# Performance work log

Measured on AMD Instinct MI355X. Metric: run time of the kernel, lower is better.

## Reference

```python
import jax, jax.numpy as jnp
import numpy as np

N_NODES = 50000
N_EDGES = 800000
IN_DIM, HID_DIM, OUT_DIM = 128, 128, 256


def _gcn_conv(x, W, b, src, dst, num_nodes):
    # PyG GCNConv: h = D^{-1/2} (A + I) D^{-1/2} X W + b (self-loops already in src/dst)
    h = x @ W  # (N, F_out)
    ones = jnp.ones(src.shape[0], dtype=h.dtype)
    deg = jax.ops.segment_sum(ones, dst, num_segments=num_nodes)
    dinv = jnp.where(deg > 0, jax.lax.rsqrt(deg), 0.0)
    norm = dinv[src] * dinv[dst]  # (E,)
    msg = h[src] * norm[:, None]  # (E, F_out) gather
    out = jax.ops.segment_sum(msg, dst, num_segments=num_nodes)  # scatter-add
    return out + b


def setup_inputs() -> dict:
    key = jax.random.key(0)
    ks = jax.random.split(key, 6)
    x = jax.random.normal(ks[0], (N_NODES, IN_DIM), dtype=jnp.float32)
    edge_index = jax.random.randint(ks[1], (2, N_EDGES), 0, N_NODES, dtype=jnp.int64)
    W1 = jax.random.normal(ks[2], (IN_DIM, HID_DIM), dtype=jnp.float32) / np.sqrt(IN_DIM)
    b1 = jnp.zeros((HID_DIM,), jnp.float32)
    W2 = jax.random.normal(ks[3], (HID_DIM, OUT_DIM), dtype=jnp.float32) / np.sqrt(HID_DIM)
    b2 = jnp.zeros((OUT_DIM,), jnp.float32)
    Wa = jax.random.normal(ks[4], (OUT_DIM, 1), dtype=jnp.float32) / np.sqrt(OUT_DIM)
    ba = jnp.zeros((1,), jnp.float32)
    return {"x": x, "edge_index": edge_index, "W1": W1, "b1": b1, "W2": W2, "b2": b2, "Wa": Wa, "ba": ba}


def reference(x, edge_index, W1, b1, W2, b2, Wa, ba):
    n = x.shape[0]
    loops = jnp.arange(n, dtype=edge_index.dtype)
    src = jnp.concatenate([edge_index[0], loops])
    dst = jnp.concatenate([edge_index[1], loops])
    h = jax.nn.relu(_gcn_conv(x, W1, b1, src, dst, n))
    # dropout is a no-op in eval mode
    node_embeddings = jax.nn.relu(_gcn_conv(h, W2, b2, src, dst, n))
    logits = node_embeddings @ Wa + ba  # (N, 1)
    attn = jax.nn.softmax(logits, axis=0)  # softmax over nodes
    graph_embedding = jnp.sum(node_embeddings * attn, axis=0, keepdims=True)  # (1, OUT_DIM)
    return (node_embeddings, graph_embedding)
```

## Files before the change

### kernel.cpp

```cpp
#include <hip/hip_runtime.h>
#include <hip/hip_fp16.h>
#include <math.h>

typedef __attribute__((ext_vector_type(8))) short bf16x8;
typedef __attribute__((ext_vector_type(4))) float f32x4;

static __device__ __forceinline__ unsigned short f2bf(float x) {
    unsigned u = __float_as_uint(x);
    unsigned r = (u + 0x7FFF + ((u >> 16) & 1)) >> 16;
    return (unsigned short)r;
}
static __device__ __forceinline__ float bf2f(unsigned short h) {
    return __uint_as_float(((unsigned)h) << 16);
}
static __device__ __forceinline__ void addh8(float a[8], uint4 v) {
    float2 f;
    f = __half22float2(*(const __half2*)&v.x); a[0] += f.x; a[1] += f.y;
    f = __half22float2(*(const __half2*)&v.y); a[2] += f.x; a[3] += f.y;
    f = __half22float2(*(const __half2*)&v.z); a[4] += f.x; a[5] += f.y;
    f = __half22float2(*(const __half2*)&v.w); a[6] += f.x; a[7] += f.y;
}
static __device__ __forceinline__ void gll16(const unsigned short* g, unsigned short* l) {
    __builtin_amdgcn_global_load_lds(
        (const __attribute__((address_space(1))) unsigned int*)(const void*)g,
        (__attribute__((address_space(3))) unsigned int*)(void*)l, 16, 0, 0);
}


__global__ __launch_bounds__(256) void count_deg_kernel(const int* __restrict__ dst, int E,
                                                        int* __restrict__ deg,
                                                        int* __restrict__ epos) {
    int e = blockIdx.x * 256 + threadIdx.x;
    if (e < E) epos[e] = atomicAdd(&deg[dst[e]], 1);
}

__global__ __launch_bounds__(256) void scan_partial_kernel(const int* __restrict__ deg, int n,
                                                           int* __restrict__ partials) {
    int idx = blockIdx.x * 1024 + threadIdx.x * 4;
    int4 v = make_int4(0, 0, 0, 0);
    if (idx + 3 < n) v = *(const int4*)(deg + idx);
    else {
        if (idx < n) v.x = deg[idx];
        if (idx + 1 < n) v.y = deg[idx + 1];
        if (idx + 2 < n) v.z = deg[idx + 2];
    }
    int s = v.x + v.y + v.z + v.w;
    for (int off = 1; off < 64; off <<= 1) s += __shfl_xor(s, off);
    __shared__ int sm[4];
    int wave = threadIdx.x >> 6;
    if ((threadIdx.x & 63) == 0) sm[wave] = s;
    __syncthreads();
    if (threadIdx.x == 0) partials[blockIdx.x] = sm[0] + sm[1] + sm[2] + sm[3];
}

__global__ __launch_bounds__(256) void scan_final_kernel(const int* __restrict__ deg, int n,
                                                         const int* __restrict__ partials, int nbk,
                                                         int* __restrict__ rowptr) {
    int idx = blockIdx.x * 1024 + threadIdx.x * 4;
    int4 v = make_int4(0, 0, 0, 0);
    if (idx + 3 < n) v = *(const int4*)(deg + idx);
    else {
        if (idx < n) v.x = deg[idx];
        if (idx + 1 < n) v.y = deg[idx + 1];
        if (idx + 2 < n) v.z = deg[idx + 2];
    }
    int tsum = v.x + v.y + v.z + v.w;
    int lane = threadIdx.x & 63, wave = threadIdx.x >> 6;
    int s = tsum;
    for (int off = 1; off < 64; off <<= 1) {
        int u = __shfl_up(s, off);
        if (lane >= off) s += u;
    }
    __shared__ int wsum[4];
    __shared__ int bb;
    if (lane == 63) wsum[wave] = s;
    if (threadIdx.x < 64) {
        int pv = (threadIdx.x < nbk) ? partials[threadIdx.x] : 0;
        int ps = pv;
        for (int off = 1; off < 64; off <<= 1) {
            int u = __shfl_up(ps, off);
            if (threadIdx.x >= off) ps += u;
        }
        if (threadIdx.x == blockIdx.x) bb = ps - pv;
        if (blockIdx.x == 0 && threadIdx.x == 63) rowptr[n] = ps;
    }
    __syncthreads();
    int base = bb;
    for (int w = 0; w < wave; ++w) base += wsum[w];
    int e0 = base + s - tsum;
    int4 o;
    o.x = e0; o.y = e0 + v.x; o.z = o.y + v.y; o.w = o.z + v.z;
    if (idx + 3 < n) *(int4*)(rowptr + idx) = o;
    else {
        if (idx < n) rowptr[idx] = o.x;
        if (idx + 1 < n) rowptr[idx + 1] = o.y;
        if (idx + 2 < n) rowptr[idx + 2] = o.z;
    }
}


__global__ __launch_bounds__(256) void prep_kernel(
    const int* __restrict__ src, const int* __restrict__ dst, const int* __restrict__ epos, int E,
    const int* __restrict__ rowptr, int* __restrict__ csrsrc, int scatterBlocks,
    const float* __restrict__ x, float* __restrict__ dinv,
    __half2* __restrict__ xs16, int n, int prescaleBlocks,
    const float* __restrict__ W1, const float* __restrict__ W2,
    unsigned short* __restrict__ w1h, unsigned short* __restrict__ w1l,
    unsigned short* __restrict__ w2h, unsigned short* __restrict__ w2l) {
    int b = blockIdx.x;
    if (b < scatterBlocks) {
        int e = b * 256 + threadIdx.x;
        if (e < E) csrsrc[rowptr[dst[e]] + epos[e]] = src[e];
    } else if (b < scatterBlocks + prescaleBlocks) {
        int node = (b - scatterBlocks) * 4 + (threadIdx.x >> 6);
        int lane = threadIdx.x & 63;
        if (node >= n) return;
        float di = rsqrtf((float)(rowptr[node + 1] - rowptr[node] + 1));
        if (lane == 0) dinv[node] = di;
        float2 v = *(const float2*)(x + (size_t)node * 128 + (lane << 1));
        xs16[(size_t)node * 64 + lane] = __floats2half2_rn(di * v.x, di * v.y);
    } else {
        int i = (b - scatterBlocks - prescaleBlocks) * 256 + threadIdx.x;
        if (i < 128 * 128) {
            int nn = i >> 7, k = i & 127;
            float v = W1[k * 128 + nn];
            unsigned short h = f2bf(v);
            int kp = (k & 64) + ((((k >> 3) & 7) ^ (nn & 7)) << 3) + (k & 7);
            w1h[nn * 128 + kp] = h;
            w1l[nn * 128 + kp] = f2bf(v - bf2f(h));
        } else if (i < 128 * 128 + 256 * 128) {
            int j = i - 128 * 128;
            int nn = j >> 7, k = j & 127;
            float v = W2[k * 256 + nn];
            unsigned short h = f2bf(v);
            int kp = (k & 64) + ((((k >> 3) & 7) ^ (nn & 7)) << 3) + (k & 7);
            w2h[nn * 128 + kp] = h;
            w2l[nn * 128 + kp] = f2bf(v - bf2f(h));
        }
    }
}


__global__ __launch_bounds__(256) void aggregate_kernel(const unsigned short* __restrict__ X16,
                                                        const float* __restrict__ dinv,
                                                        const int* __restrict__ rowptr,
                                                        const int* __restrict__ csrsrc,
                                                        unsigned short* __restrict__ outH,
                                                        unsigned short* __restrict__ outL, int n) {
    int node = blockIdx.x * 16 + (threadIdx.x >> 4);
    int sl = threadIdx.x & 15;
    if (node >= n) return;
    const uint4* Xv = (const uint4*)X16;
    float acc[8] = {0.f, 0.f, 0.f, 0.f, 0.f, 0.f, 0.f, 0.f};
    addh8(acc, Xv[(size_t)node * 16 + sl]);
    int e0 = rowptr[node];
    int e1 = rowptr[node + 1];
    int e = e0;
    for (; e + 4 <= e1; e += 4) {
        int s0 = csrsrc[e], s1 = csrsrc[e + 1], s2 = csrsrc[e + 2], s3 = csrsrc[e + 3];
        uint4 v0 = Xv[(size_t)s0 * 16 + sl];
        uint4 v1 = Xv[(size_t)s1 * 16 + sl];
        uint4 v2 = Xv[(size_t)s2 * 16 + sl];
        uint4 v3 = Xv[(size_t)s3 * 16 + sl];
        addh8(acc, v0); addh8(acc, v1); addh8(acc, v2); addh8(acc, v3);
    }
    for (; e < e1; ++e) {
        uint4 v = Xv[(size_t)csrsrc[e] * 16 + sl];
        addh8(acc, v);
    }
    float di = dinv[node];
    unsigned short h[8], l[8];
#pragma unroll
    for (int j = 0; j < 8; ++j) {
        float f = di * acc[j];
        h[j] = f2bf(f);
        l[j] = f2bf(f - bf2f(h[j]));
    }
    uint4 hv, lv;
    hv.x = (unsigned)h[0] | ((unsigned)h[1] << 16);
    hv.y = (unsigned)h[2] | ((unsigned)h[3] << 16);
    hv.z = (unsigned)h[4] | ((unsigned)h[5] << 16);
    hv.w = (unsigned)h[6] | ((unsigned)h[7] << 16);
    lv.x = (unsigned)l[0] | ((unsigned)l[1] << 16);
    lv.y = (unsigned)l[2] | ((unsigned)l[3] << 16);
    lv.z = (unsigned)l[4] | ((unsigned)l[5] << 16);
    lv.w = (unsigned)l[6] | ((unsigned)l[7] << 16);
    int pos = ((sl & 8) | ((sl & 7) ^ (node & 7))) * 8;
    *(uint4*)(outH + (size_t)node * 128 + pos) = hv;
    *(uint4*)(outL + (size_t)node * 128 + pos) = lv;
}


template <int N, bool SCALE_DINV, bool DO_LOGITS, bool OUT_F16>
__global__ __launch_bounds__(256, 2) void gemm_mfma(const unsigned short* __restrict__ Ah,
                                                    const unsigned short* __restrict__ Al,
                                                    const unsigned short* __restrict__ Bth,
                                                    const unsigned short* __restrict__ Btl,
                                                    const float* __restrict__ bias,
                                                    void* __restrict__ Cout, int M,
                                                    const float* __restrict__ dinv,
                                                    const float* __restrict__ Wa,
                                                    float* __restrict__ logits) {
    __shared__ unsigned short AsH[128 * 64];
    __shared__ unsigned short AsL[128 * 64];
    __shared__ unsigned short BsH[128 * 64];
    __shared__ unsigned short BsL[128 * 64];

    const int t = threadIdx.x;
    const int lane = t & 63;
    const int wave = t >> 6;
    const int wrow = wave >> 1;
    const int wcol = wave & 1;
    const int lq = lane >> 4;
    const int lm = lane & 15;
    const int row0 = blockIdx.x * 128;
    const int col0 = blockIdx.y * 128;

    const int lr = lane >> 3;
    const int p8 = (lane & 7) * 8;

    f32x4 acc[4][4] = {};
    float lacc[4][4] = {};

    for (int kc = 0; kc < 2; ++kc) {
        __syncthreads();
#pragma unroll
        for (int j = 0; j < 4; ++j) {
            int seg = wave * 4 + j;
            int r = seg * 8 + lr;
            size_t goA = (size_t)(row0 + r) * 128 + kc * 64 + p8;
            size_t goB = (size_t)(col0 + r) * 128 + kc * 64 + p8;
            gll16(Ah + goA, AsH + seg * 512);
            gll16(Al + goA, AsL + seg * 512);
            gll16(Bth + goB, BsH + seg * 512);
            gll16(Btl + goB, BsL + seg * 512);
        }
        __syncthreads();

#pragma unroll
        for (int ks = 0; ks < 2; ++ks) {
            bf16x8 ah[4], al[4], bh[4], bl[4];
            int gbase = ks * 4 + lq;
#pragma unroll
            for (int rt = 0; rt < 4; ++rt) {
                int ra = wrow * 64 + rt * 16 + lm;
                int off = ra * 64 + (gbase ^ (ra & 7)) * 8;
                ah[rt] = *(const bf16x8*)(AsH + off);
                al[rt] = *(const bf16x8*)(AsL + off);
            }
#pragma unroll
            for (int ct = 0; ct < 4; ++ct) {
                int nb = wcol * 64 + ct * 16 + lm;
                int off = nb * 64 + (gbase ^ (nb & 7)) * 8;
                bh[ct] = *(const bf16x8*)(BsH + off);
                bl[ct] = *(const bf16x8*)(BsL + off);
            }
#pragma unroll
            for (int rt = 0; rt < 4; ++rt)
#pragma unroll
                for (int ct = 0; ct < 4; ++ct) {
                    acc[rt][ct] = __builtin_amdgcn_mfma_f32_16x16x32_bf16(ah[rt], bh[ct], acc[rt][ct], 0, 0, 0);
                    acc[rt][ct] = __builtin_amdgcn_mfma_f32_16x16x32_bf16(al[rt], bh[ct], acc[rt][ct], 0, 0, 0);
                    acc[rt][ct] = __builtin_amdgcn_mfma_f32_16x16x32_bf16(ah[rt], bl[ct], acc[rt][ct], 0, 0, 0);
                }
        }
    }

#pragma unroll
    for (int ct = 0; ct < 4; ++ct) {
        int col = col0 + wcol * 64 + ct * 16 + lm;
        float bc = bias[col];
        float wac = DO_LOGITS ? Wa[col] : 0.f;
#pragma unroll
        for (int rt = 0; rt < 4; ++rt) {
            int rowb = row0 + wrow * 64 + rt * 16 + lq * 4;
#pragma unroll
            for (int reg = 0; reg < 4; ++reg) {
                int gr = rowb + reg;
                if (gr < M) {
                    float o = fmaxf(acc[rt][ct][reg] + bc, 0.f);
                    if (SCALE_DINV) o *= dinv[gr];
                    if (OUT_F16) ((__half*)Cout)[(size_t)gr * N + col] = __float2half(o);
                    else ((float*)Cout)[(size_t)gr * N + col] = o;
                    if (DO_LOGITS) lacc[rt][reg] += o * wac;
                }
            }
        }
    }

    if (DO_LOGITS) {
#pragma unroll
        for (int rt = 0; rt < 4; ++rt)
#pragma unroll
            for (int reg = 0; reg < 4; ++reg) {
                float s = lacc[rt][reg];
                s += __shfl_xor(s, 1);
                s += __shfl_xor(s, 2);
                s += __shfl_xor(s, 4);
                s += __shfl_xor(s, 8);
                int gr = row0 + wrow * 64 + rt * 16 + lq * 4 + reg;
                if (lm == 0 && gr < M) atomicAdd(&logits[gr], s);
            }
    }
}


__global__ __launch_bounds__(256) void maxsum_kernel(const float* __restrict__ logits, int n,
                                                     float2* __restrict__ part,
                                                     float* __restrict__ outTail) {
    if (blockIdx.x == 0) outTail[threadIdx.x] = 0.f;
    float m = -INFINITY, s = 0.f;
    for (int i = blockIdx.x * 256 + threadIdx.x; i < n; i += gridDim.x * 256) {
        float v = logits[i];
        if (v > m) { s = s * expf(m - v) + 1.f; m = v; }
        else s += expf(v - m);
    }
    __shared__ float sm[256], ss[256];
    sm[threadIdx.x] = m; ss[threadIdx.x] = s;
    __syncthreads();
    for (int off = 128; off > 0; off >>= 1) {
        if (threadIdx.x < off) {
            float m1 = sm[threadIdx.x], s1 = ss[threadIdx.x];
            float m2 = sm[threadIdx.x + off], s2 = ss[threadIdx.x + off];
            float M = fmaxf(m1, m2);
            sm[threadIdx.x] = M;
            ss[threadIdx.x] = s1 * expf(m1 - M) + s2 * expf(m2 - M);
        }
        __syncthreads();
    }
    if (threadIdx.x == 0) part[blockIdx.x] = make_float2(sm[0], ss[0]);
}

static __device__ __forceinline__ float2 merge_part(const float2* __restrict__ part, int t,
                                                    float* red2) {
    if (t < 64) {
        float2 p = part[t];
        float m = p.x, s = p.y;
        for (int off = 32; off > 0; off >>= 1) {
            float m2 = __shfl_xor(m, off);
            float s2 = __shfl_xor(s, off);
            float M = fmaxf(m, m2);
            s = s * expf(m - M) + s2 * expf(m2 - M);
            m = M;
        }
        if (t == 0) { red2[0] = m; red2[1] = s; }
    }
    __syncthreads();
    return make_float2(red2[0], red2[1]);
}

__global__ __launch_bounds__(256) void weighted_sum_kernel(const float* __restrict__ emb,
                                                           const float* __restrict__ logits,
                                                           const float2* __restrict__ part,
                                                           float* __restrict__ gpart, int n) {
    __shared__ float red2[2];
    float g = merge_part(part, threadIdx.x, red2).x;
    int wave = threadIdx.x >> 6;
    int lane = threadIdx.x & 63;
    int stride = gridDim.x * 4;
    float4 acc = make_float4(0.f, 0.f, 0.f, 0.f);
#pragma unroll 2
    for (int r = blockIdx.x * 4 + wave; r < n; r += stride) {
        float w = expf(logits[r] - g);
        float4 v = *(const float4*)(emb + (size_t)r * 256 + (lane << 2));
        acc.x += w * v.x; acc.y += w * v.y; acc.z += w * v.z; acc.w += w * v.w;
    }
    __shared__ float4 sm[256];
    sm[threadIdx.x] = acc;
    __syncthreads();
    if (wave == 0) {
        float4 a = sm[lane], b = sm[64 + lane], c = sm[128 + lane], d = sm[192 + lane];
        float4 s;
        s.x = (a.x + b.x) + (c.x + d.x);
        s.y = (a.y + b.y) + (c.y + d.y);
        s.z = (a.z + b.z) + (c.z + d.z);
        s.w = (a.w + b.w) + (c.w + d.w);
        *(float4*)(gpart + (size_t)blockIdx.x * 256 + (lane << 2)) = s;
    }
}

__global__ __launch_bounds__(256) void reduce_gpart_kernel(const float* __restrict__ gpart,
                                                           const float2* __restrict__ part,
                                                           float* __restrict__ outTail, int nb) {
    __shared__ float red2[2];
    float gsum = merge_part(part, threadIdx.x, red2).y;
    int rows = nb / gridDim.x;
    int r0 = blockIdx.x * rows;
    float s = 0.f;
    for (int r = r0; r < r0 + rows; ++r) s += gpart[(size_t)r * 256 + threadIdx.x];
    atomicAdd(&outTail[threadIdx.x], s / gsum);
}


extern "C" void kernel_launch(void* const* d_in, const int* in_sizes, int n_in,
                              void* d_out, int out_size, void* d_ws, size_t ws_size,
                              hipStream_t stream) {
    const float* x  = (const float*)d_in[0];
    const int* ei   = (const int*)d_in[1];
    const float* W1 = (const float*)d_in[2];
    const float* b1 = (const float*)d_in[3];
    const float* W2 = (const float*)d_in[4];
    const float* b2 = (const float*)d_in[5];
    const float* Wa = (const float*)d_in[6];
    float* out = (float*)d_out;

    const int n = in_sizes[0] / 128;
    const int E = in_sizes[1] / 2;
    const int* srcA = ei;
    const int* dstA = ei + E;
    const int nb = (n + 1023) / 1024;
    const int WS_BLOCKS = 1024;

    unsigned short* xs16 = (unsigned short*)d_ws;
    unsigned short* aggH = xs16 + (size_t)n * 128;
    unsigned short* aggL = aggH + (size_t)n * 128;
    unsigned short* w1h  = aggL + (size_t)n * 128;
    unsigned short* w1l  = w1h + 128 * 128;
    unsigned short* w2h  = w1l + 128 * 128;
    unsigned short* w2l  = w2h + 256 * 128;
    float* dinv   = (float*)(w2l + 256 * 128);
    float* logits = dinv + n;
    int* deg      = (int*)(logits + n);
    int* rowptr   = deg + n;
    int* partials = rowptr + n + 1;
    float2* part  = (float2*)(partials + 64);
    float* gpart  = (float*)(part + 64);
    int* epos     = (int*)(gpart + WS_BLOCKS * 256);
    int* csrsrc   = epos + E;

    hipMemsetAsync(logits, 0, sizeof(float) * (size_t)(2 * n), stream);

    count_deg_kernel<<<(E + 255) / 256, 256, 0, stream>>>(dstA, E, deg, epos);
    scan_partial_kernel<<<nb, 256, 0, stream>>>(deg, n, partials);
    scan_final_kernel<<<nb, 256, 0, stream>>>(deg, n, partials, nb, rowptr);

    int scatterBlocks = (E + 255) / 256;
    int prescaleBlocks = (n + 3) / 4;
    int wconvBlocks = (128 * 128 + 256 * 128 + 255) / 256;
    prep_kernel<<<scatterBlocks + prescaleBlocks + wconvBlocks, 256, 0, stream>>>(
        srcA, dstA, epos, E, rowptr, csrsrc, scatterBlocks,
        x, dinv, (__half2*)xs16, n, prescaleBlocks,
        W1, W2, w1h, w1l, w2h, w2l);

    int aggBlocks = (n + 15) / 16;
    int gemmRows = (n + 127) / 128;

    aggregate_kernel<<<aggBlocks, 256, 0, stream>>>(xs16, dinv, rowptr, csrsrc, aggH, aggL, n);
    gemm_mfma<128, true, false, true><<<dim3(gemmRows, 1), 256, 0, stream>>>(
        aggH, aggL, w1h, w1l, b1, xs16, n, dinv, nullptr, nullptr);
    aggregate_kernel<<<aggBlocks, 256, 0, stream>>>(xs16, dinv, rowptr, csrsrc, aggH, aggL, n);
    gemm_mfma<256, false, true, false><<<dim3(gemmRows, 2), 256, 0, stream>>>(
        aggH, aggL, w2h, w2l, b2, out, n, nullptr, Wa, logits);

    maxsum_kernel<<<64, 256, 0, stream>>>(logits, n, part, out + (size_t)n * 256);
    weighted_sum_kernel<<<WS_BLOCKS, 256, 0, stream>>>(out, logits, part, gpart, n);
    reduce_gpart_kernel<<<32, 256, 0, stream>>>(gpart, part, out + (size_t)n * 256, WS_BLOCKS);
}
```

Baseline: 291.7 us.

## Fuse neighbor aggregation into MFMA GEMM, staging aggregated rows in LDS

Each GCN layer's CSR gather-aggregate now runs inside the GEMM kernel. A 512-thread block aggregates 128 rows into split bf16 hi/lo LDS tiles, then multiplies them by weights read directly from global memory instead of staged through LDS. This removes the aggH/aggL round-trip through global memory and two kernel launches. The layer-2 GEMM now covers all 256 columns per block instead of splitting them across two blocks, so each block loads more weight data and gets less column parallelism. The gather phase also uses only four threads per node with wide per-thread accumulators, which may raise register pressure and reduce memory-level parallelism.

Result: no change. 296.8 us (+1.7%).

```diff
diff --git a/kernel.cpp b/kernel.cpp
--- a/kernel.cpp
+++ b/kernel.cpp
@@ -13,17 +13,12 @@
 static __device__ __forceinline__ float bf2f(unsigned short h) {
     return __uint_as_float(((unsigned)h) << 16);
 }
-static __device__ __forceinline__ void addh8(float a[8], uint4 v) {
+static __device__ __forceinline__ void addh8(float* a, uint4 v) {
     float2 f;
     f = __half22float2(*(const __half2*)&v.x); a[0] += f.x; a[1] += f.y;
     f = __half22float2(*(const __half2*)&v.y); a[2] += f.x; a[3] += f.y;
     f = __half22float2(*(const __half2*)&v.z); a[4] += f.x; a[5] += f.y;
     f = __half22float2(*(const __half2*)&v.w); a[6] += f.x; a[7] += f.y;
-}
-static __device__ __forceinline__ void gll16(const unsigned short* g, unsigned short* l) {
-    __builtin_amdgcn_global_load_lds(
-        (const __attribute__((address_space(1))) unsigned int*)(const void*)g,
-        (__attribute__((address_space(3))) unsigned int*)(void*)l, 16, 0, 0);
 }
 
 
@@ -125,150 +120,135 @@
             int nn = i >> 7, k = i & 127;
             float v = W1[k * 128 + nn];
             unsigned short h = f2bf(v);
-            int kp = (k & 64) + ((((k >> 3) & 7) ^ (nn & 7)) << 3) + (k & 7);
-            w1h[nn * 128 + kp] = h;
-            w1l[nn * 128 + kp] = f2bf(v - bf2f(h));
+            w1h[nn * 128 + k] = h;
+            w1l[nn * 128 + k] = f2bf(v - bf2f(h));
         } else if (i < 128 * 128 + 256 * 128) {
             int j = i - 128 * 128;
             int nn = j >> 7, k = j & 127;
             float v = W2[k * 256 + nn];
             unsigned short h = f2bf(v);
-            int kp = (k & 64) + ((((k >> 3) & 7) ^ (nn & 7)) << 3) + (k & 7);
-            w2h[nn * 128 + kp] = h;
-            w2l[nn * 128 + kp] = f2bf(v - bf2f(h));
-        }
-    }
-}
-
-
-__global__ __launch_bounds__(256) void aggregate_kernel(const unsigned short* __restrict__ X16,
-                                                        const float* __restrict__ dinv,
-                                                        const int* __restrict__ rowptr,
-                                                        const int* __restrict__ csrsrc,
-                                                        unsigned short* __restrict__ outH,
-                                                        unsigned short* __restrict__ outL, int n) {
-    int node = blockIdx.x * 16 + (threadIdx.x >> 4);
-    int sl = threadIdx.x & 15;
-    if (node >= n) return;
-    const uint4* Xv = (const uint4*)X16;
-    float acc[8] = {0.f, 0.f, 0.f, 0.f, 0.f, 0.f, 0.f, 0.f};
-    addh8(acc, Xv[(size_t)node * 16 + sl]);
-    int e0 = rowptr[node];
-    int e1 = rowptr[node + 1];
-    int e = e0;
-    for (; e + 4 <= e1; e += 4) {
-        int s0 = csrsrc[e], s1 = csrsrc[e + 1], s2 = csrsrc[e + 2], s3 = csrsrc[e + 3];
-        uint4 v0 = Xv[(size_t)s0 * 16 + sl];
-        uint4 v1 = Xv[(size_t)s1 * 16 + sl];
-        uint4 v2 = Xv[(size_t)s2 * 16 + sl];
-        uint4 v3 = Xv[(size_t)s3 * 16 + sl];
-        addh8(acc, v0); addh8(acc, v1); addh8(acc, v2); addh8(acc, v3);
-    }
-    for (; e < e1; ++e) {
-        uint4 v = Xv[(size_t)csrsrc[e] * 16 + sl];
-        addh8(acc, v);
-    }
-    float di = dinv[node];
-    unsigned short h[8], l[8];
-#pragma unroll
-    for (int j = 0; j < 8; ++j) {
-        float f = di * acc[j];
-        h[j] = f2bf(f);
-        l[j] = f2bf(f - bf2f(h[j]));
-    }
-    uint4 hv, lv;
-    hv.x = (unsigned)h[0] | ((unsigned)h[1] << 16);
-    hv.y = (unsigned)h[2] | ((unsigned)h[3] << 16);
-    hv.z = (unsigned)h[4] | ((unsigned)h[5] << 16);
-    hv.w = (unsigned)h[6] | ((unsigned)h[7] << 16);
-    lv.x = (unsigned)l[0] | ((unsigned)l[1] << 16);
-    lv.y = (unsigned)l[2] | ((unsigned)l[3] << 16);
-    lv.z = (unsigned)l[4] | ((unsigned)l[5] << 16);
-    lv.w = (unsigned)l[6] | ((unsigned)l[7] << 16);
-    int pos = ((sl & 8) | ((sl & 7) ^ (node & 7))) * 8;
-    *(uint4*)(outH + (size_t)node * 128 + pos) = hv;
-    *(uint4*)(outL + (size_t)node * 128 + pos) = lv;
-}
-
-
-template <int N, bool SCALE_DINV, bool DO_LOGITS, bool OUT_F16>
-__global__ __launch_bounds__(256, 2) void gemm_mfma(const unsigned short* __restrict__ Ah,
-                                                    const unsigned short* __restrict__ Al,
-                                                    const unsigned short* __restrict__ Bth,
-                                                    const unsigned short* __restrict__ Btl,
-                                                    const float* __restrict__ bias,
-                                                    void* __restrict__ Cout, int M,
-                                                    const float* __restrict__ dinv,
-                                                    const float* __restrict__ Wa,
-                                                    float* __restrict__ logits) {
-    __shared__ unsigned short AsH[128 * 64];
-    __shared__ unsigned short AsL[128 * 64];
-    __shared__ unsigned short BsH[128 * 64];
-    __shared__ unsigned short BsL[128 * 64];
+            w2h[nn * 128 + k] = h;
+            w2l[nn * 128 + k] = f2bf(v - bf2f(h));
+        }
+    }
+}
+
+
+template <int NCOLS, bool SCALE_DINV, bool DO_LOGITS, bool OUT_F16>
+__global__ __launch_bounds__(512, 2) void fused_gemm(
+    const unsigned short* __restrict__ X16,
+    const int* __restrict__ rowptr, const int* __restrict__ csrsrc,
+    const float* __restrict__ dinv,
+    const unsigned short* __restrict__ Bth, const unsigned short* __restrict__ Btl,
+    const float* __restrict__ bias, void* __restrict__ Cout, int M,
+    const float* __restrict__ Wa, float* __restrict__ logits) {
+    constexpr int CT = NCOLS / 64;
+    __shared__ unsigned short AsH[128 * 128];
+    __shared__ unsigned short AsL[128 * 128];
 
     const int t = threadIdx.x;
+    const int row0 = blockIdx.x * 128;
+
+    {
+        const int nl = t >> 2;
+        const int sub = t & 3;
+        const int row = row0 + nl;
+        float acc[32];
+#pragma unroll
+        for (int i = 0; i < 32; ++i) acc[i] = 0.f;
+        float di = 0.f;
+        if (row < M) {
+            const uint4* __restrict__ Xv = (const uint4*)X16;
+            size_t sb = (size_t)row * 16 + sub * 4;
+            uint4 v0 = Xv[sb], v1 = Xv[sb + 1], v2 = Xv[sb + 2], v3 = Xv[sb + 3];
+            addh8(acc, v0); addh8(acc + 8, v1); addh8(acc + 16, v2); addh8(acc + 24, v3);
+            int e1 = rowptr[row + 1];
+            int e = rowptr[row];
+            for (; e + 2 <= e1; e += 2) {
+                int s0 = csrsrc[e], s1 = csrsrc[e + 1];
+                size_t b0 = (size_t)s0 * 16 + sub * 4;
+                size_t b1 = (size_t)s1 * 16 + sub * 4;
+                uint4 a0 = Xv[b0], a1 = Xv[b0 + 1], a2 = Xv[b0 + 2], a3 = Xv[b0 + 3];
+                uint4 c0 = Xv[b1], c1 = Xv[b1 + 1], c2 = Xv[b1 + 2], c3 = Xv[b1 + 3];
+                addh8(acc, a0); addh8(acc + 8, a1); addh8(acc + 16, a2); addh8(acc + 24, a3);
+                addh8(acc, c0); addh8(acc + 8, c1); addh8(acc + 16, c2); addh8(acc + 24, c3);
+            }
+            if (e < e1) {
+                size_t b0 = (size_t)csrsrc[e] * 16 + sub * 4;
+                uint4 a0 = Xv[b0], a1 = Xv[b0 + 1], a2 = Xv[b0 + 2], a3 = Xv[b0 + 3];
+                addh8(acc, a0); addh8(acc + 8, a1); addh8(acc + 16, a2); addh8(acc + 24, a3);
+            }
+            di = dinv[row];
+        }
+#pragma unroll
+        for (int j = 0; j < 4; ++j) {
+            int ga = sub * 4 + j;
+            int off = nl * 128 + (ga >> 3) * 64 + (((ga & 7) ^ (nl & 7)) << 3);
+            unsigned short h[8], l[8];
+#pragma unroll
+            for (int q = 0; q < 8; ++q) {
+                float f = di * acc[j * 8 + q];
+                h[q] = f2bf(f);
+                l[q] = f2bf(f - bf2f(h[q]));
+            }
+            uint4 hv, lv;
+            hv.x = (unsigned)h[0] | ((unsigned)h[1] << 16);
+            hv.y = (unsigned)h[2] | ((unsigned)h[3] << 16);
+            hv.z = (unsigned)h[4] | ((unsigned)h[5] << 16);
+            hv.w = (unsigned)h[6] | ((unsigned)h[7] << 16);
+            lv.x = (unsigned)l[0] | ((unsigned)l[1] << 16);
+            lv.y = (unsigned)l[2] | ((unsigned)l[3] << 16);
+            lv.z = (unsigned)l[4] | ((unsigned)l[5] << 16);
+            lv.w = (unsigned)l[6] | ((unsigned)l[7] << 16);
+            *(uint4*)(AsH + off) = hv;
+            *(uint4*)(AsL + off) = lv;
+        }
+    }
+    __syncthreads();
+
     const int lane = t & 63;
     const int wave = t >> 6;
-    const int wrow = wave >> 1;
-    const int wcol = wave & 1;
+    const int wrow = wave >> 2;
+    const int wcol = wave & 3;
     const int lq = lane >> 4;
     const int lm = lane & 15;
-    const int row0 = blockIdx.x * 128;
-    const int col0 = blockIdx.y * 128;
-
-    const int lr = lane >> 3;
-    const int p8 = (lane & 7) * 8;
-
-    f32x4 acc[4][4] = {};
+
+    f32x4 acc2[4][CT] = {};
     float lacc[4][4] = {};
 
-    for (int kc = 0; kc < 2; ++kc) {
-        __syncthreads();
-#pragma unroll
-        for (int j = 0; j < 4; ++j) {
-            int seg = wave * 4 + j;
-            int r = seg * 8 + lr;
-            size_t goA = (size_t)(row0 + r) * 128 + kc * 64 + p8;
-            size_t goB = (size_t)(col0 + r) * 128 + kc * 64 + p8;
-            gll16(Ah + goA, AsH + seg * 512);
-            gll16(Al + goA, AsL + seg * 512);
-            gll16(Bth + goB, BsH + seg * 512);
-            gll16(Btl + goB, BsL + seg * 512);
-        }
-        __syncthreads();
-
+#pragma unroll
+    for (int kc = 0; kc < 2; ++kc)
 #pragma unroll
         for (int ks = 0; ks < 2; ++ks) {
-            bf16x8 ah[4], al[4], bh[4], bl[4];
-            int gbase = ks * 4 + lq;
+            const int gbase = ks * 4 + lq;
+            bf16x8 ah[4], al[4], bh[CT], bl[CT];
 #pragma unroll
             for (int rt = 0; rt < 4; ++rt) {
                 int ra = wrow * 64 + rt * 16 + lm;
-                int off = ra * 64 + (gbase ^ (ra & 7)) * 8;
+                int off = ra * 128 + kc * 64 + ((gbase ^ (ra & 7)) << 3);
                 ah[rt] = *(const bf16x8*)(AsH + off);
                 al[rt] = *(const bf16x8*)(AsL + off);
             }
 #pragma unroll
-            for (int ct = 0; ct < 4; ++ct) {
-                int nb = wcol * 64 + ct * 16 + lm;
-                int off = nb * 64 + (gbase ^ (nb & 7)) * 8;
-                bh[ct] = *(const bf16x8*)(BsH + off);
-                bl[ct] = *(const bf16x8*)(BsL + off);
+            for (int ct = 0; ct < CT; ++ct) {
+                int col = wcol * (16 * CT) + ct * 16 + lm;
+                size_t bo = (size_t)col * 128 + kc * 64 + gbase * 8;
+                bh[ct] = *(const bf16x8*)(Bth + bo);
+                bl[ct] = *(const bf16x8*)(Btl + bo);
             }
 #pragma unroll
             for (int rt = 0; rt < 4; ++rt)
 #pragma unroll
-                for (int ct = 0; ct < 4; ++ct) {
-                    acc[rt][ct] = __builtin_amdgcn_mfma_f32_16x16x32_bf16(ah[rt], bh[ct], acc[rt][ct], 0, 0, 0);
-                    acc[rt][ct] = __builtin_amdgcn_mfma_f32_16x16x32_bf16(al[rt], bh[ct], acc[rt][ct], 0, 0, 0);
-                    acc[rt][ct] = __builtin_amdgcn_mfma_f32_16x16x32_bf16(ah[rt], bl[ct], acc[rt][ct], 0, 0, 0);
+                for (int ct = 0; ct < CT; ++ct) {
+                    acc2[rt][ct] = __builtin_amdgcn_mfma_f32_16x16x32_bf16(ah[rt], bh[ct], acc2[rt][ct], 0, 0, 0);
+                    acc2[rt][ct] = __builtin_amdgcn_mfma_f32_16x16x32_bf16(al[rt], bh[ct], acc2[rt][ct], 0, 0, 0);
+                    acc2[rt][ct] = __builtin_amdgcn_mfma_f32_16x16x32_bf16(ah[rt], bl[ct], acc2[rt][ct], 0, 0, 0);
                 }
         }
-    }
-
-#pragma unroll
-    for (int ct = 0; ct < 4; ++ct) {
-        int col = col0 + wcol * 64 + ct * 16 + lm;
+
+#pragma unroll
+    for (int ct = 0; ct < CT; ++ct) {
+        int col = wcol * (16 * CT) + ct * 16 + lm;
         float bc = bias[col];
         float wac = DO_LOGITS ? Wa[col] : 0.f;
 #pragma unroll
@@ -278,10 +258,10 @@
             for (int reg = 0; reg < 4; ++reg) {
                 int gr = rowb + reg;
                 if (gr < M) {
-                    float o = fmaxf(acc[rt][ct][reg] + bc, 0.f);
+                    float o = fmaxf(acc2[rt][ct][reg] + bc, 0.f);
                     if (SCALE_DINV) o *= dinv[gr];
-                    if (OUT_F16) ((__half*)Cout)[(size_t)gr * N + col] = __float2half(o);
-                    else ((float*)Cout)[(size_t)gr * N + col] = o;
+                    if (OUT_F16) ((__half*)Cout)[(size_t)gr * NCOLS + col] = __float2half(o);
+                    else ((float*)Cout)[(size_t)gr * NCOLS + col] = o;
                     if (DO_LOGITS) lacc[rt][reg] += o * wac;
                 }
             }
@@ -412,9 +392,8 @@
     const int WS_BLOCKS = 1024;
 
     unsigned short* xs16 = (unsigned short*)d_ws;
-    unsigned short* aggH = xs16 + (size_t)n * 128;
-    unsigned short* aggL = aggH + (size_t)n * 128;
-    unsigned short* w1h  = aggL + (size_t)n * 128;
+    unsigned short* h16  = xs16 + (size_t)n * 128;
+    unsigned short* w1h  = h16 + (size_t)n * 128;
     unsigned short* w1l  = w1h + 128 * 128;
     unsigned short* w2h  = w1l + 128 * 128;
     unsigned short* w2l  = w2h + 256 * 128;
@@ -442,15 +421,12 @@
         x, dinv, (__half2*)xs16, n, prescaleBlocks,
         W1, W2, w1h, w1l, w2h, w2l);
 
-    int aggBlocks = (n + 15) / 16;
     int gemmRows = (n + 127) / 128;
 
-    aggregate_kernel<<<aggBlocks, 256, 0, stream>>>(xs16, dinv, rowptr, csrsrc, aggH, aggL, n);
-    gemm_mfma<128, true, false, true><<<dim3(gemmRows, 1), 256, 0, stream>>>(
-        aggH, aggL, w1h, w1l, b1, xs16, n, dinv, nullptr, nullptr);
-    aggregate_kernel<<<aggBlocks, 256, 0, stream>>>(xs16, dinv, rowptr, csrsrc, aggH, aggL, n);
-    gemm_mfma<256, false, true, false><<<dim3(gemmRows, 2), 256, 0, stream>>>(
-        aggH, aggL, w2h, w2l, b2, out, n, nullptr, Wa, logits);
+    fused_gemm<128, true, false, true><<<gemmRows, 512, 0, stream>>>(
+        xs16, rowptr, csrsrc, dinv, w1h, w1l, b1, h16, n, nullptr, nullptr);
+    fused_gemm<256, false, true, false><<<gemmRows, 512, 0, stream>>>(
+        h16, rowptr, csrsrc, dinv, w2h, w2l, b2, out, n, Wa, logits);
 
     maxsum_kernel<<<64, 256, 0, stream>>>(logits, n, part, out + (size_t)n * 256);
     weighted_sum_kernel<<<WS_BLOCKS, 256, 0, stream>>>(out, logits, part, gpart, n);
```

## Split fp16 feature table into column chunks and aggregate chunk-by-chunk

Applied to the files above, without the earlier changes.

The fp16 node-feature table is stored as four column-chunk planes of 32 halves each, written both by the prescale step and by the layer-1 GEMM epilogue. Aggregation now runs as four separate launches, one per chunk, so each gathered working set (about 3.2 MB) can stay resident in L2/LLC during the random neighbor gathers. Each launch re-reads the CSR arrays, and the index loads are marked nontemporal and unrolled by eight. The cost is four times the CSR index traffic, more kernel launches, and a strided GEMM output write pattern.

Measured after the change: 350.1 us. +20.0%, slower.

```diff
diff --git a/kernel.cpp b/kernel.cpp
--- a/kernel.cpp
+++ b/kernel.cpp
@@ -13,7 +13,7 @@
 static __device__ __forceinline__ float bf2f(unsigned short h) {
     return __uint_as_float(((unsigned)h) << 16);
 }
-static __device__ __forceinline__ void addh8(float a[8], uint4 v) {
+static __device__ __forceinline__ void addh8(float* a, uint4 v) {
     float2 f;
     f = __half22float2(*(const __half2*)&v.x); a[0] += f.x; a[1] += f.y;
     f = __half22float2(*(const __half2*)&v.y); a[2] += f.x; a[3] += f.y;
@@ -103,7 +103,7 @@
     const int* __restrict__ src, const int* __restrict__ dst, const int* __restrict__ epos, int E,
     const int* __restrict__ rowptr, int* __restrict__ csrsrc, int scatterBlocks,
     const float* __restrict__ x, float* __restrict__ dinv,
-    __half2* __restrict__ xs16, int n, int prescaleBlocks,
+    __half2* __restrict__ xs16c, int n, int prescaleBlocks,
     const float* __restrict__ W1, const float* __restrict__ W2,
     unsigned short* __restrict__ w1h, unsigned short* __restrict__ w1l,
     unsigned short* __restrict__ w2h, unsigned short* __restrict__ w2l) {
@@ -118,7 +118,8 @@
         float di = rsqrtf((float)(rowptr[node + 1] - rowptr[node] + 1));
         if (lane == 0) dinv[node] = di;
         float2 v = *(const float2*)(x + (size_t)node * 128 + (lane << 1));
-        xs16[(size_t)node * 64 + lane] = __floats2half2_rn(di * v.x, di * v.y);
+        xs16c[((size_t)(lane >> 4) * n + node) * 16 + (lane & 15)] =
+            __floats2half2_rn(di * v.x, di * v.y);
     } else {
         int i = (b - scatterBlocks - prescaleBlocks) * 256 + threadIdx.x;
         if (i < 128 * 128) {
@@ -141,40 +142,61 @@
 }
 
 
-__global__ __launch_bounds__(256) void aggregate_kernel(const unsigned short* __restrict__ X16,
-                                                        const float* __restrict__ dinv,
-                                                        const int* __restrict__ rowptr,
-                                                        const int* __restrict__ csrsrc,
-                                                        unsigned short* __restrict__ outH,
-                                                        unsigned short* __restrict__ outL, int n) {
-    int node = blockIdx.x * 16 + (threadIdx.x >> 4);
-    int sl = threadIdx.x & 15;
+__global__ __launch_bounds__(256) void agg_chunk_kernel(
+    const unsigned short* __restrict__ X16c, const int* __restrict__ rowptr,
+    const int* __restrict__ csrsrc, const float* __restrict__ dinv,
+    unsigned short* __restrict__ outH, unsigned short* __restrict__ outL,
+    int n, int chunk) {
+    int node = blockIdx.x * 64 + (threadIdx.x >> 2);
+    int sub = threadIdx.x & 3;
     if (node >= n) return;
-    const uint4* Xv = (const uint4*)X16;
+    const uint4* __restrict__ Xv = (const uint4*)X16c + (size_t)chunk * n * 4;
     float acc[8] = {0.f, 0.f, 0.f, 0.f, 0.f, 0.f, 0.f, 0.f};
-    addh8(acc, Xv[(size_t)node * 16 + sl]);
-    int e0 = rowptr[node];
+    addh8(acc, Xv[(size_t)node * 4 + sub]);
+    int e = rowptr[node];
     int e1 = rowptr[node + 1];
-    int e = e0;
+    for (; e + 8 <= e1; e += 8) {
+        int s0 = __builtin_nontemporal_load(csrsrc + e);
+        int s1 = __builtin_nontemporal_load(csrsrc + e + 1);
+        int s2 = __builtin_nontemporal_load(csrsrc + e + 2);
+        int s3 = __builtin_nontemporal_load(csrsrc + e + 3);
+        int s4 = __builtin_nontemporal_load(csrsrc + e + 4);
+        int s5 = __builtin_nontemporal_load(csrsrc + e + 5);
+        int s6 = __builtin_nontemporal_load(csrsrc + e + 6);
+        int s7 = __builtin_nontemporal_load(csrsrc + e + 7);
+        uint4 v0 = Xv[(size_t)s0 * 4 + sub];
+        uint4 v1 = Xv[(size_t)s1 * 4 + sub];
+        uint4 v2 = Xv[(size_t)s2 * 4 + sub];
+        uint4 v3 = Xv[(size_t)s3 * 4 + sub];
+        uint4 v4 = Xv[(size_t)s4 * 4 + sub];
+        uint4 v5 = Xv[(size_t)s5 * 4 + sub];
+        uint4 v6 = Xv[(size_t)s6 * 4 + sub];
+        uint4 v7 = Xv[(size_t)s7 * 4 + sub];
+        addh8(acc, v0); addh8(acc, v1); addh8(acc, v2); addh8(acc, v3);
+        addh8(acc, v4); addh8(acc, v5); addh8(acc, v6); addh8(acc, v7);
+    }
     for (; e + 4 <= e1; e += 4) {
-        int s0 = csrsrc[e], s1 = csrsrc[e + 1], s2 = csrsrc[e + 2], s3 = csrsrc[e + 3];
-        uint4 v0 = Xv[(size_t)s0 * 16 + sl];
-        uint4 v1 = Xv[(size_t)s1 * 16 + sl];
-        uint4 v2 = Xv[(size_t)s2 * 16 + sl];
-        uint4 v3 = Xv[(size_t)s3 * 16 + sl];
+        int s0 = __builtin_nontemporal_load(csrsrc + e);
+        int s1 = __builtin_nontemporal_load(csrsrc + e + 1);
+        int s2 = __builtin_nontemporal_load(csrsrc + e + 2);
+        int s3 = __builtin_nontemporal_load(csrsrc + e + 3);
+        uint4 v0 = Xv[(size_t)s0 * 4 + sub];
+        uint4 v1 = Xv[(size_t)s1 * 4 + sub];
+        uint4 v2 = Xv[(size_t)s2 * 4 + sub];
+        uint4 v3 = Xv[(size_t)s3 * 4 + sub];
         addh8(acc, v0); addh8(acc, v1); addh8(acc, v2); addh8(acc, v3);
     }
     for (; e < e1; ++e) {
-        uint4 v = Xv[(size_t)csrsrc[e] * 16 + sl];
-        addh8(acc, v);
+        int s0 = __builtin_nontemporal_load(csrsrc + e);
+        addh8(acc, Xv[(size_t)s0 * 4 + sub]);
     }
     float di = dinv[node];
     unsigned short h[8], l[8];
 #pragma unroll
-    for (int j = 0; j < 8; ++j) {
-        float f = di * acc[j];
-        h[j] = f2bf(f);
-        l[j] = f2bf(f - bf2f(h[j]));
+    for (int q = 0; q < 8; ++q) {
+        float f = di * acc[q];
+        h[q] = f2bf(f);
+        l[q] = f2bf(f - bf2f(h[q]));
     }
     uint4 hv, lv;
     hv.x = (unsigned)h[0] | ((unsigned)h[1] << 16);
@@ -185,7 +207,8 @@
     lv.y = (unsigned)l[2] | ((unsigned)l[3] << 16);
     lv.z = (unsigned)l[4] | ((unsigned)l[5] << 16);
     lv.w = (unsigned)l[6] | ((unsigned)l[7] << 16);
-    int pos = ((sl & 8) | ((sl & 7) ^ (node & 7))) * 8;
+    int ga = chunk * 4 + sub;
+    int pos = ((ga & 8) | ((ga & 7) ^ (node & 7))) * 8;
     *(uint4*)(outH + (size_t)node * 128 + pos) = hv;
     *(uint4*)(outL + (size_t)node * 128 + pos) = lv;
 }
@@ -280,7 +303,8 @@
                 if (gr < M) {
                     float o = fmaxf(acc[rt][ct][reg] + bc, 0.f);
                     if (SCALE_DINV) o *= dinv[gr];
-                    if (OUT_F16) ((__half*)Cout)[(size_t)gr * N + col] = __float2half(o);
+                    if (OUT_F16)
+                        ((__half*)Cout)[((size_t)(col >> 5) * M + gr) * 32 + (col & 31)] = __float2half(o);
                     else ((float*)Cout)[(size_t)gr * N + col] = o;
                     if (DO_LOGITS) lacc[rt][reg] += o * wac;
                 }
@@ -411,13 +435,13 @@
     const int nb = (n + 1023) / 1024;
     const int WS_BLOCKS = 1024;
 
-    unsigned short* xs16 = (unsigned short*)d_ws;
-    unsigned short* aggH = xs16 + (size_t)n * 128;
-    unsigned short* aggL = aggH + (size_t)n * 128;
-    unsigned short* w1h  = aggL + (size_t)n * 128;
-    unsigned short* w1l  = w1h + 128 * 128;
-    unsigned short* w2h  = w1l + 128 * 128;
-    unsigned short* w2l  = w2h + 256 * 128;
+    unsigned short* xs16c = (unsigned short*)d_ws;
+    unsigned short* aggH  = xs16c + (size_t)n * 128;
+    unsigned short* aggL  = aggH + (size_t)n * 128;
+    unsigned short* w1h   = aggL + (size_t)n * 128;
+    unsigned short* w1l   = w1h + 128 * 128;
+    unsigned short* w2h   = w1l + 128 * 128;
+    unsigned short* w2l   = w2h + 256 * 128;
     float* dinv   = (float*)(w2l + 256 * 128);
     float* logits = dinv + n;
     int* deg      = (int*)(logits + n);
@@ -439,16 +463,19 @@
     int wconvBlocks = (128 * 128 + 256 * 128 + 255) / 256;
     prep_kernel<<<scatterBlocks + prescaleBlocks + wconvBlocks, 256, 0, stream>>>(
         srcA, dstA, epos, E, rowptr, csrsrc, scatterBlocks,
-        x, dinv, (__half2*)xs16, n, prescaleBlocks,
+        x, dinv, (__half2*)xs16c, n, prescaleBlocks,
         W1, W2, w1h, w1l, w2h, w2l);
 
-    int aggBlocks = (n + 15) / 16;
+    int NB = (n + 63) / 64;
     int gemmRows = (n + 127) / 128;
 
-    aggregate_kernel<<<aggBlocks, 256, 0, stream>>>(xs16, dinv, rowptr, csrsrc, aggH, aggL, n);
+    for (int c = 0; c < 4; ++c)
+        agg_chunk_kernel<<<NB, 256, 0, stream>>>(xs16c, rowptr, csrsrc, dinv, aggH, aggL, n, c);
     gemm_mfma<128, true, false, true><<<dim3(gemmRows, 1), 256, 0, stream>>>(
-        aggH, aggL, w1h, w1l, b1, xs16, n, dinv, nullptr, nullptr);
-    aggregate_kernel<<<aggBlocks, 256, 0, stream>>>(xs16, dinv, rowptr, csrsrc, aggH, aggL, n);
+        aggH, aggL, w1h, w1l, b1, xs16c, n, dinv, nullptr, nullptr);
+
+    for (int c = 0; c < 4; ++c)
+        agg_chunk_kernel<<<NB, 256, 0, stream>>>(xs16c, rowptr, csrsrc, dinv, aggH, aggL, n, c);
     gemm_mfma<256, false, true, false><<<dim3(gemmRows, 2), 256, 0, stream>>>(
         aggH, aggL, w2h, w2l, b2, out, n, nullptr, Wa, logits);
 
```
